# Kernel optimization log

Hardware: AMD Instinct MI355X
Metric: run time of the kernel (lower is better)

Reference implementation:

```python
import jax, jax.numpy as jnp
import numpy as np

B, LT, D, N, H = 16, 512, 1024, 4096, 16
LN_EPS = 1e-5


def setup_inputs() -> dict:
    key = jax.random.key(0)
    ks = jax.random.split(key, 10)
    s = 0.02
    struct_token = jax.random.normal(ks[0], (N, D), dtype=jnp.float32)
    text_token = jax.random.normal(ks[1], (B, LT, D), dtype=jnp.float32)
    # contiguous, sorted segment ids: 256 struct tokens per batch element
    struct_batch = jnp.repeat(jnp.arange(B, dtype=jnp.int32), N // B)
    return {
        "struct_token": struct_token,
        "text_token": text_token,
        "in_proj_w": jax.random.normal(ks[2], (3 * D, D), dtype=jnp.float32) * s,
        "in_proj_b": jnp.zeros((3 * D,), jnp.float32),
        "attn_out_w": jax.random.normal(ks[3], (D, D), dtype=jnp.float32) * s,
        "attn_out_b": jnp.zeros((D,), jnp.float32),
        "ln_g": jnp.ones((D,), jnp.float32),
        "ln_b": jnp.zeros((D,), jnp.float32),
        "proj_w": jax.random.normal(ks[4], (D, D), dtype=jnp.float32) * s,
        "proj_b": jnp.zeros((D,), jnp.float32),
        "struct_batch": struct_batch,
        "L_max": N // B,
    }


def reference(struct_token, text_token, in_proj_w, in_proj_b, attn_out_w,
              attn_out_b, ln_g, ln_b, proj_w, proj_b, struct_batch, L_max):
    Bq = text_token.shape[0]
    Dm = struct_token.shape[-1]
    dh = Dm // H
    Ntok = struct_token.shape[0]

    # ---- ragged pad-pack (struct_batch is sorted/contiguous per segment) ----
    counts = jnp.bincount(struct_batch, length=Bq)                 # [B]
    starts = jnp.concatenate([jnp.zeros((1,), counts.dtype),
                              jnp.cumsum(counts)[:-1]])            # [B]
    pos = jnp.arange(Ntok) - starts[struct_batch]                  # [N] position in segment
    padded = jnp.zeros((Bq, L_max, Dm), struct_token.dtype)
    padded = padded.at[struct_batch, pos].set(struct_token)        # [B, Ls, D]

    # ---- nn.MultiheadAttention (batch_first): Q=padded, K=V=text ----
    wq, wk, wv = in_proj_w[:Dm], in_proj_w[Dm:2 * Dm], in_proj_w[2 * Dm:]
    bq, bk, bv = in_proj_b[:Dm], in_proj_b[Dm:2 * Dm], in_proj_b[2 * Dm:]
    q = (padded @ wq.T + bq).reshape(Bq, L_max, H, dh)
    k = (text_token @ wk.T + bk).reshape(Bq, -1, H, dh)
    v = (text_token @ wv.T + bv).reshape(Bq, -1, H, dh)
    scores = jnp.einsum('bqhd,bkhd->bhqk', q, k) / jnp.sqrt(jnp.float32(dh))
    attn = jax.nn.softmax(scores, axis=-1)
    ctx = jnp.einsum('bhqk,bkhd->bqhd', attn, v).reshape(Bq, L_max, Dm)
    fused = ctx @ attn_out_w.T + attn_out_b                        # [B, Ls, D]

    # ---- LayerNorm + output projection ----
    mu = fused.mean(-1, keepdims=True)
    var = fused.var(-1, keepdims=True)
    fused = (fused - mu) * jax.lax.rsqrt(var + LN_EPS) * ln_g + ln_b
    fused = fused @ proj_w.T + proj_b

    # ---- unpack valid tokens + scatter-mean over segments ----
    tok = fused[struct_batch, pos]                                 # [N, D]
    seg_sum = jax.ops.segment_sum(tok, struct_batch, num_segments=Bq)
    return seg_sum / jnp.maximum(counts, 1)[:, None].astype(seg_sum.dtype)
```

## Files before the change

kernel.cpp:

```cpp
#include <hip/hip_runtime.h>

constexpr int B  = 16;
constexpr int LT = 512;
constexpr int D  = 1024;
constexpr int N  = 4096;
constexpr int H  = 16;
constexpr int DH = D / H;
constexpr int LMAX = N / B;
constexpr float LN_EPS = 1e-5f;

typedef short  s16x8 __attribute__((ext_vector_type(8)));
typedef float  f32x4 __attribute__((ext_vector_type(4)));

__device__ __forceinline__ unsigned short f2bf(float x) {
    unsigned int u = __float_as_uint(x);
    unsigned int r = (u + 0x7fffu + ((u >> 16) & 1u)) >> 16;
    return (unsigned short)r;
}
__device__ __forceinline__ float bf2f(unsigned short u) {
    return __uint_as_float((unsigned int)u << 16);
}

__device__ __forceinline__ void load_lds16(const void* g, void* l) {
    __builtin_amdgcn_global_load_lds(
        (const __attribute__((address_space(1))) unsigned int*)g,
        (__attribute__((address_space(3))) unsigned int*)l, 16, 0, 0);
}

__global__ __launch_bounds__(256) void cast3_prep(
        const float* __restrict__ x0, unsigned short* __restrict__ y0, int n0,
        const float* __restrict__ x1, unsigned short* __restrict__ y1, int n1,
        const float* __restrict__ x2, unsigned short* __restrict__ y2, int n2,
        const int* __restrict__ sb, int* __restrict__ counts, int* __restrict__ starts) {
    __shared__ int s_counts[B];
    int t = threadIdx.x;
    if (blockIdx.x == 6144) {
        if (t < B) s_counts[t] = 0;
        __syncthreads();
        for (int i = t; i < N; i += 256) atomicAdd(&s_counts[sb[i]], 1);
        __syncthreads();
        if (t == 0) {
            int run = 0;
            for (int b = 0; b < B; b++) { starts[b] = run; run += s_counts[b]; }
        }
        if (t < B) counts[t] = s_counts[t];
        return;
    }
    long long i = (long long)(blockIdx.x * 256 + t) * 8;
    const float* x; unsigned short* y;
    if (i < n0)                { x = x0 + i; y = y0 + i; }
    else if (i < (long long)n0 + n1) { long long j = i - n0; x = x1 + j; y = y1 + j; }
    else if (i < (long long)n0 + n1 + n2) { long long j = i - n0 - n1; x = x2 + j; y = y2 + j; }
    else return;
    float4 a = *(const float4*)x;
    float4 b = *(const float4*)(x + 4);
    ushort4 o1, o2;
    o1.x = f2bf(a.x); o1.y = f2bf(a.y); o1.z = f2bf(a.z); o1.w = f2bf(a.w);
    o2.x = f2bf(b.x); o2.y = f2bf(b.y); o2.z = f2bf(b.z); o2.w = f2bf(b.w);
    *(ushort4*)y = o1;
    *(ushort4*)(y + 4) = o2;
}

__global__ void scatter_full(const float* __restrict__ st,
                             const int* __restrict__ counts,
                             const int* __restrict__ starts,
                             unsigned short* __restrict__ padded) {
    int p = blockIdx.x, b = blockIdx.y;
    int d = threadIdx.x * 4;
    size_t off = ((size_t)(b * LMAX + p)) * D + d;
    ushort4 o = {0, 0, 0, 0};
    if (p < counts[b]) {
        float4 v = *(const float4*)&st[(size_t)(starts[b] + p) * D + d];
        o.x = f2bf(v.x); o.y = f2bf(v.y); o.z = f2bf(v.z); o.w = f2bf(v.w);
    }
    *(ushort4*)&padded[off] = o;
}

template<typename Epi>
__device__ __forceinline__ void gemm8ph(const unsigned short* __restrict__ A,
                                        const unsigned short* __restrict__ W,
                                        int K, int kbeg, int kend, int m0, int n0,
                                        unsigned short* __restrict__ As,
                                        unsigned short* __restrict__ Bs,
                                        Epi&& epi) {
    const int tid  = threadIdx.x;
    const int lane = tid & 63;
    const int wid  = tid >> 6;
    const int wr   = wid >> 1;
    const int wc   = wid & 1;
    const int fm   = lane & 15;
    const int quad = lane >> 4;
    const int NK   = (kend - kbeg) >> 6;

    f32x4 acc[4][4];
#pragma unroll
    for (int i = 0; i < 4; i++)
#pragma unroll
        for (int j = 0; j < 4; j++) acc[i][j] = (f32x4){0.f, 0.f, 0.f, 0.f};

    auto stageA = [&](int s) {
        const int k0 = kbeg + (s << 6);
        unsigned short* Ad = As + (s & 1) * 16384;
#pragma unroll
        for (int r = 0; r < 4; r++) {
            int ci  = r * 512 + tid;
            int row = ci >> 3;
            int sg  = (ci & 7) ^ (row & 7);
            load_lds16(A + (size_t)(m0 + row) * K + k0 + sg * 8, Ad + ci * 8);
        }
    };
    auto stageB = [&](int s) {
        const int k0 = kbeg + (s << 6);
        unsigned short* Bd = Bs + (s & 1) * 8192;
#pragma unroll
        for (int r = 0; r < 2; r++) {
            int ci  = r * 512 + tid;
            int row = ci >> 3;
            int sg  = (ci & 7) ^ (row & 7);
            load_lds16(W + (size_t)(n0 + row) * K + k0 + sg * 8, Bd + ci * 8);
        }
    };

    stageA(0);
    stageB(0);

    for (int s = 0; s < NK; s++) {
        const unsigned short* Ab = As + (s & 1) * 16384;
        const unsigned short* Bb = Bs + (s & 1) * 8192;

        __builtin_amdgcn_s_barrier();
        __builtin_amdgcn_sched_barrier(0);
        if (s + 1 < NK) { stageA(s + 1); stageB(s + 1); }
        if (s + 1 < NK) asm volatile("s_waitcnt vmcnt(6)" ::: "memory");
        else            asm volatile("s_waitcnt vmcnt(0)" ::: "memory");
        __builtin_amdgcn_s_barrier();
        __builtin_amdgcn_sched_barrier(0);

        s16x8 af[4][2], bf0[2][2];
#pragma unroll
        for (int i = 0; i < 4; i++) {
            int row = wr * 64 + i * 16 + fm;
#pragma unroll
            for (int kk = 0; kk < 2; kk++) {
                int sl = (kk * 4 + quad) ^ (row & 7);
                af[i][kk] = *(const s16x8*)&Ab[row * 64 + sl * 8];
            }
        }
#pragma unroll
        for (int j = 0; j < 2; j++) {
            int row = wc * 64 + j * 16 + fm;
#pragma unroll
            for (int kk = 0; kk < 2; kk++) {
                int sl = (kk * 4 + quad) ^ (row & 7);
                bf0[j][kk] = *(const s16x8*)&Bb[row * 64 + sl * 8];
            }
        }
        asm volatile("s_waitcnt lgkmcnt(0)" ::: "memory");
        __builtin_amdgcn_sched_barrier(0);
        __builtin_amdgcn_s_setprio(1);
#pragma unroll
        for (int kk = 0; kk < 2; kk++)
#pragma unroll
            for (int i = 0; i < 4; i++)
#pragma unroll
                for (int j = 0; j < 2; j++)
                    acc[i][j] = __builtin_amdgcn_mfma_f32_16x16x32_bf16(af[i][kk], bf0[j][kk], acc[i][j], 0, 0, 0);
        __builtin_amdgcn_s_setprio(0);

        s16x8 bf1[2][2];
#pragma unroll
        for (int j = 0; j < 2; j++) {
            int row = wc * 64 + (2 + j) * 16 + fm;
#pragma unroll
            for (int kk = 0; kk < 2; kk++) {
                int sl = (kk * 4 + quad) ^ (row & 7);
                bf1[j][kk] = *(const s16x8*)&Bb[row * 64 + sl * 8];
            }
        }
        asm volatile("s_waitcnt lgkmcnt(0)" ::: "memory");
        __builtin_amdgcn_sched_barrier(0);
        __builtin_amdgcn_s_setprio(1);
#pragma unroll
        for (int kk = 0; kk < 2; kk++)
#pragma unroll
            for (int i = 0; i < 4; i++)
#pragma unroll
                for (int j = 0; j < 2; j++)
                    acc[i][2 + j] = __builtin_amdgcn_mfma_f32_16x16x32_bf16(af[i][kk], bf1[j][kk], acc[i][2 + j], 0, 0, 0);
        __builtin_amdgcn_s_setprio(0);
    }

    const int fr = quad * 4;
#pragma unroll
    for (int i = 0; i < 4; i++)
#pragma unroll
        for (int j = 0; j < 4; j++) {
            int row = m0 + wr * 64 + i * 16 + fr;
            int col = n0 + wc * 64 + j * 16 + fm;
#pragma unroll
            for (int r = 0; r < 4; r++)
                epi(row + r, col, acc[i][j][r]);
        }
}

__global__ __launch_bounds__(512, 2) void qkv_fused(const unsigned short* __restrict__ padded,
                                                    const unsigned short* __restrict__ text,
                                                    const unsigned short* __restrict__ wqkv,
                                                    const float* __restrict__ bqkv,
                                                    unsigned short* __restrict__ qpack,
                                                    unsigned short* __restrict__ kpack,
                                                    unsigned short* __restrict__ vpack) {
    __shared__ __align__(16) unsigned short As[2 * 16384];
    __shared__ __align__(16) unsigned short Bs[2 * 8192];
    int orig = blockIdx.x;
    int id = (orig & 7) * 80 + (orig >> 3);
    if (id < 128) {
        int mt = id >> 3, nt = id & 7;
        gemm8ph(padded, wqkv, D, 0, D, mt * 256, nt * 128, As, Bs,
            [&](int mm, int col, float v) {
                float val = v + bqkv[col];
                int b = mm >> 8, q = mm & 255;
                int h = col >> 6, d = col & 63;
                qpack[(size_t)(b * H + h) * 16384 + (d >> 3) * 2048 + q * 8 + (d & 7)] = f2bf(val);
            });
    } else if (id < 384) {
        int f = id - 128;
        int mt = f >> 3, nt = f & 7;
        gemm8ph(text, wqkv + (size_t)D * D, D, 0, D, mt * 256, nt * 128, As, Bs,
            [&](int mm, int col, float v) {
                float val = v + bqkv[D + col];
                int b = mm >> 9, key = mm & 511;
                int h = col >> 6, d = col & 63;
                kpack[(size_t)(b * H + h) * 32768 + (d >> 3) * 4096 + key * 8 + (d & 7)] = f2bf(val);
            });
    } else {
        int f = id - 384;
        int mt = f >> 6, nt = f & 63;
        gemm8ph(wqkv + 2 * (size_t)D * D, text, D, 0, D, mt * 256, nt * 128, As, Bs,
            [&](int mm, int col, float v) {
                float val = v + bqkv[2 * D + mm];
                int h = mm >> 6, d = mm & 63;
                int b = col >> 9, key = col & 511;
                vpack[(size_t)(b * H + h) * 32768 + (key >> 3) * 512 + d * 8 + (key & 7)] = f2bf(val);
            });
    }
}

__global__ __launch_bounds__(512, 2) void gemm_bf2(const unsigned short* __restrict__ A,
                                                   const unsigned short* __restrict__ W,
                                                   unsigned short* __restrict__ C0,
                                                   unsigned short* __restrict__ C1,
                                                   int Nn, int K) {
    __shared__ __align__(16) unsigned short As[2 * 16384];
    __shared__ __align__(16) unsigned short Bs[2 * 8192];
    int orig = blockIdx.x;
    int id = (orig & 7) * 32 + (orig >> 3);
    int kh = id >> 7;
    int f  = id & 127;
    int mt = f >> 3, nt = f & 7;
    unsigned short* C = kh ? C1 : C0;
    gemm8ph(A, W, K, kh * 512, (kh + 1) * 512, mt * 256, nt * 128, As, Bs,
        [&](int mm, int col, float v) {
            C[(size_t)mm * Nn + col] = f2bf(v);
        });
}

constexpr int PKW = 72;

__global__ __launch_bounds__(512) void attn_mfma(const unsigned short* __restrict__ qpack,
                                                 const unsigned short* __restrict__ kpack,
                                                 const unsigned short* __restrict__ vpack,
                                                 unsigned short* __restrict__ ctx) {
    __shared__ __align__(16) unsigned short KV[16384];
    __shared__ __align__(16) unsigned short Ps[8 * 16 * PKW];

    const int tid = threadIdx.x;
    const int lane = tid & 63;
    const int wv = tid >> 6;
    const int fm = lane & 15;
    const int quad = lane >> 4;
    const int h = blockIdx.x, b = blockIdx.y, half = blockIdx.z;
    const int q0 = half * 128 + wv * 16;

    const unsigned short* qp = qpack + (size_t)(b * H + h) * 16384;
    const unsigned short* kp = kpack + (size_t)(b * H + h) * 32768;
    const unsigned short* vp = vpack + (size_t)(b * H + h) * 32768;

    const s16x8 aq0 = *(const s16x8*)&qp[quad * 2048 + (q0 + fm) * 8];
    const s16x8 aq1 = *(const s16x8*)&qp[(4 + quad) * 2048 + (q0 + fm) * 8];

    f32x4 sc[32];

    for (int kc = 0; kc < 2; kc++) {
        __syncthreads();
#pragma unroll
        for (int it = 0; it < 4; it++) {
            int f = it * 512 + tid;
            load_lds16(kp + (f >> 8) * 4096 + kc * 2048 + (f & 255) * 8, KV + f * 8);
        }
        __syncthreads();
#pragma unroll
        for (int t = 0; t < 16; t++) {
            s16x8 bk0 = *(const s16x8*)&KV[quad * 2048 + (t * 16 + fm) * 8];
            s16x8 bk1 = *(const s16x8*)&KV[(4 + quad) * 2048 + (t * 16 + fm) * 8];
            f32x4 a = (f32x4){0.f, 0.f, 0.f, 0.f};
            a = __builtin_amdgcn_mfma_f32_16x16x32_bf16(aq0, bk0, a, 0, 0, 0);
            a = __builtin_amdgcn_mfma_f32_16x16x32_bf16(aq1, bk1, a, 0, 0, 0);
            sc[kc * 16 + t] = a;
        }
    }

    const float scale = 0.125f;
    float mx[4], l[4], inv[4];
#pragma unroll
    for (int r = 0; r < 4; r++) {
        float m = sc[0][r];
#pragma unroll
        for (int t = 1; t < 32; t++) m = fmaxf(m, sc[t][r]);
        mx[r] = m;
    }
#pragma unroll
    for (int o = 1; o < 16; o <<= 1)
#pragma unroll
        for (int r = 0; r < 4; r++) mx[r] = fmaxf(mx[r], __shfl_xor(mx[r], o));
#pragma unroll
    for (int r = 0; r < 4; r++) l[r] = 0.f;
#pragma unroll
    for (int t = 0; t < 32; t++)
#pragma unroll
        for (int r = 0; r < 4; r++) {
            float e = __expf((sc[t][r] - mx[r]) * scale);
            sc[t][r] = e;
            l[r] += e;
        }
#pragma unroll
    for (int o = 1; o < 16; o <<= 1)
#pragma unroll
        for (int r = 0; r < 4; r++) l[r] += __shfl_xor(l[r], o);
#pragma unroll
    for (int r = 0; r < 4; r++) inv[r] = 1.f / l[r];

    f32x4 co[4];
#pragma unroll
    for (int n = 0; n < 4; n++) co[n] = (f32x4){0.f, 0.f, 0.f, 0.f};
    unsigned short* Pw = Ps + wv * (16 * PKW);

    for (int vc = 0; vc < 2; vc++) {
        __syncthreads();
#pragma unroll
        for (int it = 0; it < 4; it++) {
            int f = it * 512 + tid;
            load_lds16(vp + vc * 16384 + f * 8, KV + f * 8);
        }
        __syncthreads();
        for (int cs = 0; cs < 4; cs++) {
            int c = vc * 4 + cs;
#pragma unroll
            for (int tt = 0; tt < 4; tt++)
#pragma unroll
                for (int r = 0; r < 4; r++)
                    Pw[(quad * 4 + r) * PKW + tt * 16 + fm] = f2bf(sc[c * 4 + tt][r]);
#pragma unroll
            for (int s = 0; s < 2; s++) {
                s16x8 ap = *(const s16x8*)&Pw[fm * PKW + s * 32 + quad * 8];
#pragma unroll
                for (int n = 0; n < 4; n++) {
                    s16x8 bv = *(const s16x8*)&KV[(cs * 8 + s * 4 + quad) * 512 + (n * 16 + fm) * 8];
                    co[n] = __builtin_amdgcn_mfma_f32_16x16x32_bf16(ap, bv, co[n], 0, 0, 0);
                }
            }
        }
    }

    const size_t obase = (size_t)(b * LMAX + q0) * D + h * DH;
#pragma unroll
    for (int n = 0; n < 4; n++)
#pragma unroll
        for (int r = 0; r < 4; r++)
            ctx[obase + (size_t)(quad * 4 + r) * D + n * 16 + fm] = f2bf(co[n][r] * inv[r]);
}

__global__ __launch_bounds__(256) void lnmean_kernel(const unsigned short* __restrict__ f1a,
                                                     const unsigned short* __restrict__ f1b,
                                                     const float* __restrict__ bo,
                                                     const float* __restrict__ g,
                                                     const float* __restrict__ bb,
                                                     const int* __restrict__ counts,
                                                     float* __restrict__ msum) {
    int b = blockIdx.x;
    int t = threadIdx.x;
    int wv = t >> 6, lane = t & 63;
    int cnt = counts[b];
    int s0 = blockIdx.y * 32 + wv * 8;
    int s1 = min(cnt, s0 + 8);

    float4 gg[4], bv[4], bo4[4];
#pragma unroll
    for (int c = 0; c < 4; c++) {
        gg[c]  = *(const float4*)&g[c * 256 + lane * 4];
        bv[c]  = *(const float4*)&bb[c * 256 + lane * 4];
        bo4[c] = *(const float4*)&bo[c * 256 + lane * 4];
    }
    float4 acc[4];
#pragma unroll
    for (int c = 0; c < 4; c++) acc[c] = (float4){0.f, 0.f, 0.f, 0.f};

    for (int s = s0; s < s1; s++) {
        size_t rbase = ((size_t)(b * LMAX + s)) * D;
        float4 v[4];
        float sm = 0.f, ss = 0.f;
#pragma unroll
        for (int c = 0; c < 4; c++) {
            ushort4 ua = *(const ushort4*)&f1a[rbase + c * 256 + lane * 4];
            ushort4 ub = *(const ushort4*)&f1b[rbase + c * 256 + lane * 4];
            v[c].x = bf2f(ua.x) + bf2f(ub.x) + bo4[c].x;
            v[c].y = bf2f(ua.y) + bf2f(ub.y) + bo4[c].y;
            v[c].z = bf2f(ua.z) + bf2f(ub.z) + bo4[c].z;
            v[c].w = bf2f(ua.w) + bf2f(ub.w) + bo4[c].w;
            sm += v[c].x + v[c].y + v[c].z + v[c].w;
            ss += v[c].x * v[c].x + v[c].y * v[c].y + v[c].z * v[c].z + v[c].w * v[c].w;
        }
#pragma unroll
        for (int o = 32; o; o >>= 1) { sm += __shfl_xor(sm, o); ss += __shfl_xor(ss, o); }
        float mu = sm * (1.f / D);
        float var = ss * (1.f / D) - mu * mu;
        float r = rsqrtf(var + LN_EPS);
#pragma unroll
        for (int c = 0; c < 4; c++) {
            acc[c].x += (v[c].x - mu) * r * gg[c].x + bv[c].x;
            acc[c].y += (v[c].y - mu) * r * gg[c].y + bv[c].y;
            acc[c].z += (v[c].z - mu) * r * gg[c].z + bv[c].z;
            acc[c].w += (v[c].w - mu) * r * gg[c].w + bv[c].w;
        }
    }
    float inv = 1.f / (float)max(cnt, 1);
#pragma unroll
    for (int c = 0; c < 4; c++) {
        int base = b * D + c * 256 + lane * 4;
        atomicAdd(&msum[base + 0], acc[c].x * inv);
        atomicAdd(&msum[base + 1], acc[c].y * inv);
        atomicAdd(&msum[base + 2], acc[c].z * inv);
        atomicAdd(&msum[base + 3], acc[c].w * inv);
    }
}

__global__ __launch_bounds__(256) void tproj_kernel(const float* __restrict__ msum,
                                                    const float* __restrict__ W,
                                                    const float* __restrict__ bias,
                                                    float* __restrict__ out) {
    int lane = threadIdx.x & 63;
    int n = blockIdx.x * 4 + (threadIdx.x >> 6);
    float4 wr[4];
#pragma unroll
    for (int i = 0; i < 4; i++)
        wr[i] = *(const float4*)&W[(size_t)n * D + i * 256 + lane * 4];
    float bn = bias[n];
    for (int b = 0; b < B; b++) {
        float s = 0.f;
#pragma unroll
        for (int i = 0; i < 4; i++) {
            float4 m4 = *(const float4*)&msum[(size_t)b * D + i * 256 + lane * 4];
            s += m4.x * wr[i].x + m4.y * wr[i].y + m4.z * wr[i].z + m4.w * wr[i].w;
        }
#pragma unroll
        for (int o = 32; o; o >>= 1) s += __shfl_xor(s, o);
        if (lane == 0) out[(size_t)b * D + n] = s + bn;
    }
}

extern "C" void kernel_launch(void* const* d_in, const int* in_sizes, int n_in,
                              void* d_out, int out_size, void* d_ws, size_t ws_size,
                              hipStream_t stream) {
    const float* struct_token = (const float*)d_in[0];
    const float* text_token   = (const float*)d_in[1];
    const float* in_proj_w    = (const float*)d_in[2];
    const float* in_proj_b    = (const float*)d_in[3];
    const float* attn_out_w   = (const float*)d_in[4];
    const float* attn_out_b   = (const float*)d_in[5];
    const float* ln_g         = (const float*)d_in[6];
    const float* ln_b         = (const float*)d_in[7];
    const float* proj_w       = (const float*)d_in[8];
    const float* proj_b       = (const float*)d_in[9];
    const int*   sb           = (const int*)d_in[10];
    float* out = (float*)d_out;

    const size_t MQ  = (size_t)B * LMAX;
    const size_t MKV = (size_t)B * LT;

    char* p = (char*)d_ws;
    unsigned short* padded_b = (unsigned short*)p;  p += MQ * D * 2;
    unsigned short* text_b   = (unsigned short*)p;  p += MKV * D * 2;
    unsigned short* wqkv_b   = (unsigned short*)p;  p += (size_t)3 * D * D * 2;
    unsigned short* wattn_b  = (unsigned short*)p;  p += (size_t)D * D * 2;
    unsigned short* qpack    = (unsigned short*)p;  p += MQ * D * 2;
    unsigned short* kpack    = (unsigned short*)p;  p += MKV * D * 2;
    unsigned short* vpack    = (unsigned short*)p;  p += MKV * D * 2;
    unsigned short* ctx_b    = (unsigned short*)p;  p += MQ * D * 2;
    unsigned short* f1a      = (unsigned short*)p;  p += MQ * D * 2;
    unsigned short* f1b      = (unsigned short*)p;  p += MQ * D * 2;
    float* msum = (float*)p;  p += (size_t)B * D * 4;
    int* counts = (int*)p;  p += B * 4;
    int* starts = (int*)p;  p += B * 4;

    hipMemsetAsync(msum, 0, (size_t)B * D * 4, stream);

    cast3_prep<<<6145, 256, 0, stream>>>(
        text_token, text_b, (int)(MKV * D),
        in_proj_w,  wqkv_b, 3 * D * D,
        attn_out_w, wattn_b, D * D,
        sb, counts, starts);

    scatter_full<<<dim3(LMAX, B), 256, 0, stream>>>(struct_token, counts, starts, padded_b);

    qkv_fused<<<640, 512, 0, stream>>>(padded_b, text_b, wqkv_b, in_proj_b,
                                       qpack, kpack, vpack);

    attn_mfma<<<dim3(H, B, 2), 512, 0, stream>>>(qpack, kpack, vpack, ctx_b);

    gemm_bf2<<<256, 512, 0, stream>>>(ctx_b, wattn_b, f1a, f1b, D, D);

    lnmean_kernel<<<dim3(B, 8), 256, 0, stream>>>(f1a, f1b, attn_out_b, ln_g, ln_b, counts, msum);

    tproj_kernel<<<256, 256, 0, stream>>>(msum, proj_w, proj_b, out);
}
```

Before: 267.7 us.

## Halve GEMM K-step to 32 and double occupancy with smaller LDS tiles

The shared bf16 GEMM helper now stages a 32-wide K slice per iteration instead of 64, halving the LDS footprint per block (48KB instead of 96KB). The launch bounds rise from 2 to 4 blocks per CU for the QKV and split-K GEMMs, so more waves can hide memory latency. Global/LDS addresses are precomputed outside the loop and the MFMA phases are merged into one 4x4 batch. The cost is twice as many barriers and pipeline iterations per tile, with less MFMA work between syncs, and a tighter register budget that could cause spills.

Result: faster. 261.0 us (-2.5%).

```diff
diff --git a/kernel.cpp b/kernel.cpp
--- a/kernel.cpp
+++ b/kernel.cpp
@@ -77,12 +77,12 @@
 }
 
 template<typename Epi>
-__device__ __forceinline__ void gemm8ph(const unsigned short* __restrict__ A,
-                                        const unsigned short* __restrict__ W,
-                                        int K, int kbeg, int kend, int m0, int n0,
-                                        unsigned short* __restrict__ As,
-                                        unsigned short* __restrict__ Bs,
-                                        Epi&& epi) {
+__device__ __forceinline__ void gemm32(const unsigned short* __restrict__ A,
+                                       const unsigned short* __restrict__ W,
+                                       int K, int kbeg, int kend, int m0, int n0,
+                                       unsigned short* __restrict__ As,
+                                       unsigned short* __restrict__ Bs,
+                                       Epi&& epi) {
     const int tid  = threadIdx.x;
     const int lane = tid & 63;
     const int wid  = tid >> 6;
@@ -90,7 +90,7 @@
     const int wc   = wid & 1;
     const int fm   = lane & 15;
     const int quad = lane >> 4;
-    const int NK   = (kend - kbeg) >> 6;
+    const int NK   = (kend - kbeg) >> 5;
 
     f32x4 acc[4][4];
 #pragma unroll
@@ -98,95 +98,56 @@
 #pragma unroll
         for (int j = 0; j < 4; j++) acc[i][j] = (f32x4){0.f, 0.f, 0.f, 0.f};
 
-    auto stageA = [&](int s) {
-        const int k0 = kbeg + (s << 6);
-        unsigned short* Ad = As + (s & 1) * 16384;
-#pragma unroll
-        for (int r = 0; r < 4; r++) {
-            int ci  = r * 512 + tid;
-            int row = ci >> 3;
-            int sg  = (ci & 7) ^ (row & 7);
-            load_lds16(A + (size_t)(m0 + row) * K + k0 + sg * 8, Ad + ci * 8);
-        }
-    };
-    auto stageB = [&](int s) {
-        const int k0 = kbeg + (s << 6);
-        unsigned short* Bd = Bs + (s & 1) * 8192;
-#pragma unroll
-        for (int r = 0; r < 2; r++) {
-            int ci  = r * 512 + tid;
-            int row = ci >> 3;
-            int sg  = (ci & 7) ^ (row & 7);
-            load_lds16(W + (size_t)(n0 + row) * K + k0 + sg * 8, Bd + ci * 8);
-        }
-    };
-
-    stageA(0);
-    stageB(0);
+    const int rA0 = tid >> 2,          sA0 = (tid & 3) ^ (rA0 & 3);
+    const int rA1 = (tid + 512) >> 2,  sA1 = (tid & 3) ^ (rA1 & 3);
+    const int rB  = tid >> 2,          sB  = (tid & 3) ^ (rB & 3);
+    const unsigned short* gA0 = A + (size_t)(m0 + rA0) * K + kbeg + sA0 * 8;
+    const unsigned short* gA1 = A + (size_t)(m0 + rA1) * K + kbeg + sA1 * 8;
+    const unsigned short* gB  = W + (size_t)(n0 + rB ) * K + kbeg + sB  * 8;
+    unsigned short* lA0 = As + (size_t)tid * 8;
+    unsigned short* lA1 = As + (size_t)(tid + 512) * 8;
+    unsigned short* lB  = Bs + (size_t)tid * 8;
+
+    const int sl8 = (quad ^ (fm & 3)) * 8;
+    int offA[4], offB[4];
+#pragma unroll
+    for (int i = 0; i < 4; i++) offA[i] = (wr * 64 + i * 16 + fm) * 32 + sl8;
+#pragma unroll
+    for (int j = 0; j < 4; j++) offB[j] = (wc * 64 + j * 16 + fm) * 32 + sl8;
+
+    load_lds16(gA0, lA0);
+    load_lds16(gA1, lA1);
+    load_lds16(gB , lB );
 
     for (int s = 0; s < NK; s++) {
-        const unsigned short* Ab = As + (s & 1) * 16384;
-        const unsigned short* Bb = Bs + (s & 1) * 8192;
-
-        __builtin_amdgcn_s_barrier();
-        __builtin_amdgcn_sched_barrier(0);
-        if (s + 1 < NK) { stageA(s + 1); stageB(s + 1); }
-        if (s + 1 < NK) asm volatile("s_waitcnt vmcnt(6)" ::: "memory");
-        else            asm volatile("s_waitcnt vmcnt(0)" ::: "memory");
-        __builtin_amdgcn_s_barrier();
-        __builtin_amdgcn_sched_barrier(0);
-
-        s16x8 af[4][2], bf0[2][2];
-#pragma unroll
-        for (int i = 0; i < 4; i++) {
-            int row = wr * 64 + i * 16 + fm;
-#pragma unroll
-            for (int kk = 0; kk < 2; kk++) {
-                int sl = (kk * 4 + quad) ^ (row & 7);
-                af[i][kk] = *(const s16x8*)&Ab[row * 64 + sl * 8];
-            }
-        }
-#pragma unroll
-        for (int j = 0; j < 2; j++) {
-            int row = wc * 64 + j * 16 + fm;
-#pragma unroll
-            for (int kk = 0; kk < 2; kk++) {
-                int sl = (kk * 4 + quad) ^ (row & 7);
-                bf0[j][kk] = *(const s16x8*)&Bb[row * 64 + sl * 8];
-            }
-        }
-        asm volatile("s_waitcnt lgkmcnt(0)" ::: "memory");
-        __builtin_amdgcn_sched_barrier(0);
+        const int go = (s + 1) << 5;
+        const int ab = (s & 1) << 13;
+        const int bb = (s & 1) << 12;
+        asm volatile("s_barrier" ::: "memory");
+        if (s + 1 < NK) {
+            const int ab2 = ((s + 1) & 1) << 13;
+            const int bb2 = ((s + 1) & 1) << 12;
+            load_lds16(gA0 + go, lA0 + ab2);
+            load_lds16(gA1 + go, lA1 + ab2);
+            load_lds16(gB  + go, lB  + bb2);
+            asm volatile("s_waitcnt vmcnt(3)" ::: "memory");
+        } else {
+            asm volatile("s_waitcnt vmcnt(0)" ::: "memory");
+        }
+        asm volatile("s_barrier" ::: "memory");
+
+        s16x8 af[4], bf[4];
+#pragma unroll
+        for (int i = 0; i < 4; i++) af[i] = *(const s16x8*)&As[ab + offA[i]];
+#pragma unroll
+        for (int j = 0; j < 4; j++) bf[j] = *(const s16x8*)&Bs[bb + offB[j]];
+
         __builtin_amdgcn_s_setprio(1);
 #pragma unroll
-        for (int kk = 0; kk < 2; kk++)
-#pragma unroll
-            for (int i = 0; i < 4; i++)
-#pragma unroll
-                for (int j = 0; j < 2; j++)
-                    acc[i][j] = __builtin_amdgcn_mfma_f32_16x16x32_bf16(af[i][kk], bf0[j][kk], acc[i][j], 0, 0, 0);
-        __builtin_amdgcn_s_setprio(0);
-
-        s16x8 bf1[2][2];
-#pragma unroll
-        for (int j = 0; j < 2; j++) {
-            int row = wc * 64 + (2 + j) * 16 + fm;
-#pragma unroll
-            for (int kk = 0; kk < 2; kk++) {
-                int sl = (kk * 4 + quad) ^ (row & 7);
-                bf1[j][kk] = *(const s16x8*)&Bb[row * 64 + sl * 8];
-            }
-        }
-        asm volatile("s_waitcnt lgkmcnt(0)" ::: "memory");
-        __builtin_amdgcn_sched_barrier(0);
-        __builtin_amdgcn_s_setprio(1);
-#pragma unroll
-        for (int kk = 0; kk < 2; kk++)
-#pragma unroll
-            for (int i = 0; i < 4; i++)
-#pragma unroll
-                for (int j = 0; j < 2; j++)
-                    acc[i][2 + j] = __builtin_amdgcn_mfma_f32_16x16x32_bf16(af[i][kk], bf1[j][kk], acc[i][2 + j], 0, 0, 0);
+        for (int i = 0; i < 4; i++)
+#pragma unroll
+            for (int j = 0; j < 4; j++)
+                acc[i][j] = __builtin_amdgcn_mfma_f32_16x16x32_bf16(af[i], bf[j], acc[i][j], 0, 0, 0);
         __builtin_amdgcn_s_setprio(0);
     }
 
@@ -203,20 +164,20 @@
         }
 }
 
-__global__ __launch_bounds__(512, 2) void qkv_fused(const unsigned short* __restrict__ padded,
+__global__ __launch_bounds__(512, 4) void qkv_fused(const unsigned short* __restrict__ padded,
                                                     const unsigned short* __restrict__ text,
                                                     const unsigned short* __restrict__ wqkv,
                                                     const float* __restrict__ bqkv,
                                                     unsigned short* __restrict__ qpack,
                                                     unsigned short* __restrict__ kpack,
                                                     unsigned short* __restrict__ vpack) {
-    __shared__ __align__(16) unsigned short As[2 * 16384];
-    __shared__ __align__(16) unsigned short Bs[2 * 8192];
+    __shared__ __align__(16) unsigned short As[2 * 8192];
+    __shared__ __align__(16) unsigned short Bs[2 * 4096];
     int orig = blockIdx.x;
     int id = (orig & 7) * 80 + (orig >> 3);
     if (id < 128) {
         int mt = id >> 3, nt = id & 7;
-        gemm8ph(padded, wqkv, D, 0, D, mt * 256, nt * 128, As, Bs,
+        gemm32(padded, wqkv, D, 0, D, mt * 256, nt * 128, As, Bs,
             [&](int mm, int col, float v) {
                 float val = v + bqkv[col];
                 int b = mm >> 8, q = mm & 255;
@@ -226,7 +187,7 @@
     } else if (id < 384) {
         int f = id - 128;
         int mt = f >> 3, nt = f & 7;
-        gemm8ph(text, wqkv + (size_t)D * D, D, 0, D, mt * 256, nt * 128, As, Bs,
+        gemm32(text, wqkv + (size_t)D * D, D, 0, D, mt * 256, nt * 128, As, Bs,
             [&](int mm, int col, float v) {
                 float val = v + bqkv[D + col];
                 int b = mm >> 9, key = mm & 511;
@@ -236,7 +197,7 @@
     } else {
         int f = id - 384;
         int mt = f >> 6, nt = f & 63;
-        gemm8ph(wqkv + 2 * (size_t)D * D, text, D, 0, D, mt * 256, nt * 128, As, Bs,
+        gemm32(wqkv + 2 * (size_t)D * D, text, D, 0, D, mt * 256, nt * 128, As, Bs,
             [&](int mm, int col, float v) {
                 float val = v + bqkv[2 * D + mm];
                 int h = mm >> 6, d = mm & 63;
@@ -246,20 +207,20 @@
     }
 }
 
-__global__ __launch_bounds__(512, 2) void gemm_bf2(const unsigned short* __restrict__ A,
+__global__ __launch_bounds__(512, 4) void gemm_bf2(const unsigned short* __restrict__ A,
                                                    const unsigned short* __restrict__ W,
                                                    unsigned short* __restrict__ C0,
                                                    unsigned short* __restrict__ C1,
                                                    int Nn, int K) {
-    __shared__ __align__(16) unsigned short As[2 * 16384];
-    __shared__ __align__(16) unsigned short Bs[2 * 8192];
+    __shared__ __align__(16) unsigned short As[2 * 8192];
+    __shared__ __align__(16) unsigned short Bs[2 * 4096];
     int orig = blockIdx.x;
     int id = (orig & 7) * 32 + (orig >> 3);
     int kh = id >> 7;
     int f  = id & 127;
     int mt = f >> 3, nt = f & 7;
     unsigned short* C = kh ? C1 : C0;
-    gemm8ph(A, W, K, kh * 512, (kh + 1) * 512, mt * 256, nt * 128, As, Bs,
+    gemm32(A, W, K, kh * 512, (kh + 1) * 512, mt * 256, nt * 128, As, Bs,
         [&](int mm, int col, float v) {
             C[(size_t)mm * Nn + col] = f2bf(v);
         });
```
